# Performance work log

Hardware: AMD Instinct MI355X
Metric: run time of the kernel (lower is better)

The kernel has to match this reference:

```python
import jax, jax.numpy as jnp
import numpy as np

IN_F, RED, WID, CLS, T = 700, 256, 4096, 20, 100


def _q4(W):
    # per-tensor symmetric INT4 STE: value is quantized, grad is identity
    scale = jnp.maximum(jnp.abs(W).max() / 7.0, 1e-8)
    return W + jax.lax.stop_gradient(jnp.round(W / scale) * scale - W)


def setup_inputs() -> dict:
    key = jax.random.key(0)
    ks = jax.random.split(key, 12)
    B = 64
    x = jax.random.normal(ks[0], (B, T, IN_F), dtype=jnp.float32)
    latent = jax.random.uniform(ks[1], (T,), dtype=jnp.float32)
    spatial_W = jax.random.normal(ks[2], (RED, IN_F), jnp.float32) / np.sqrt(IN_F)
    spatial_b = jnp.zeros((RED,), jnp.float32)
    conv_W = jax.random.normal(ks[3], (RED, RED, 5), jnp.float32) / np.sqrt(RED * 5)
    conv_b = jnp.zeros((RED,), jnp.float32)
    fc1_W = jax.random.normal(ks[4], (WID, RED), jnp.float32) / np.sqrt(RED)
    fc1_b = jnp.zeros((WID,), jnp.float32)
    fc2_W = jax.random.normal(ks[5], (CLS, WID), jnp.float32) / np.sqrt(WID)
    fc2_b = jnp.zeros((CLS,), jnp.float32)
    gain = jnp.asarray(1.0, jnp.float32)
    return {"x": x, "latent": latent, "spatial_W": spatial_W, "spatial_b": spatial_b,
            "conv_W": conv_W, "conv_b": conv_b, "fc1_W": fc1_W, "fc1_b": fc1_b,
            "fc2_W": fc2_W, "fc2_b": fc2_b, "gain": gain}


def _compute_drive(x, latent, spatial_W, spatial_b, conv_W, conv_b, fc1_W, fc1_b, gain):
    # spatial projection (INT4 STE linear) + relu : (B,T,RED)
    xp = jax.nn.relu(jnp.einsum("btf,rf->btr", x, _q4(spatial_W)) + spatial_b)
    # temporal conv1d over T, padding=2 (same), channels RED->RED
    xc = jax.lax.conv_general_dilated(
        xp.transpose(0, 2, 1), conv_W, window_strides=(1,), padding=[(2, 2)],
        dimension_numbers=("NCH", "OIH", "NCH"))
    conv_out = jax.nn.relu(xc + conv_b[None, :, None]).transpose(0, 2, 1)  # (B,T,RED)
    spatial_act = jax.nn.softplus(jnp.einsum("btr,wr->btw", conv_out, _q4(fc1_W)) + fc1_b)
    return spatial_act * latent[None, :, None] * jnp.abs(gain)  # (B,T,WID)


def reference(x, latent, spatial_W, spatial_b, conv_W, conv_b, fc1_W, fc1_b, fc2_W, fc2_b, gain):
    drive = _compute_drive(x, latent, spatial_W, spatial_b, conv_W, conv_b, fc1_W, fc1_b, gain)
    # Poisson spike sampling with straight-through estimator, then clamp at 1
    pois = jax.random.poisson(jax.random.key(42), jax.lax.stop_gradient(drive)).astype(drive.dtype)
    spikes = drive + jax.lax.stop_gradient(pois - drive)
    spikes = jnp.minimum(spikes, 1.0)
    # decay-weighted temporal reduction over T
    decay = jnp.exp(jnp.linspace(-2.0, 0.0, T)).astype(drive.dtype)
    weighted = jnp.einsum("btw,t->bw", spikes, decay)  # (B,WID)
    # dropout in eval mode = identity
    logits = weighted @ _q4(fc2_W).T + fc2_b  # (B,CLS)
    return (logits, spikes, drive)
```

## Files before the change

kernel.cpp:

```cpp
#include <hip/hip_runtime.h>
#include <stdint.h>

#define B 64
#define T 100
#define IN_F 700
#define RED 256
#define WID 4096
#define CLS 20
#define BT (B*T)
#define NELEM (BT*WID)
#define LOGITS_OFF 0
#define SPIKES_OFF (B*CLS)
#define DRIVE_OFF (SPIKES_OFF + NELEM)

#define WS_SLOTS 0
#define WS_W2Q 16
#define WS_XP  (WS_W2Q + CLS*WID)
#define WS_CO  (WS_XP + BT*RED)
#define WS_WEIGHTED (WS_CO + BT*RED)

#define SC_WST 0
#define SC_CWT (SC_WST + IN_F*RED)

__host__ __device__ __forceinline__ uint32_t rotl32(uint32_t v, int r) {
  return (v << r) | (v >> (32 - r));
}

__host__ __device__ __forceinline__ void threefry2x32(uint32_t k0, uint32_t k1,
                                                      uint32_t x0, uint32_t x1,
                                                      uint32_t& o0, uint32_t& o1) {
  uint32_t k2 = k0 ^ k1 ^ 0x1BD11BDAu;
  x0 += k0; x1 += k1;
#define TF_R(r) { x0 += x1; x1 = rotl32(x1, (r)); x1 ^= x0; }
  TF_R(13) TF_R(15) TF_R(26) TF_R(6)
  x0 += k1; x1 += k2 + 1u;
  TF_R(17) TF_R(29) TF_R(16) TF_R(24)
  x0 += k2; x1 += k0 + 2u;
  TF_R(13) TF_R(15) TF_R(26) TF_R(6)
  x0 += k0; x1 += k1 + 3u;
  TF_R(17) TF_R(29) TF_R(16) TF_R(24)
  x0 += k1; x1 += k2 + 4u;
  TF_R(13) TF_R(15) TF_R(26) TF_R(6)
  x0 += k2; x1 += k0 + 5u;
#undef TF_R
  o0 = x0; o1 = x1;
}

__global__ void absmax_kernel(const float* __restrict__ w, int n, uint32_t* slot) {
  __shared__ uint32_t sm[256];
  uint32_t m = 0u;
  for (int i = blockIdx.x * 256 + threadIdx.x; i < n; i += gridDim.x * 256)
    m = max(m, __float_as_uint(fabsf(w[i])));
  sm[threadIdx.x] = m;
  __syncthreads();
  for (int s = 128; s > 0; s >>= 1) {
    if (threadIdx.x < s) sm[threadIdx.x] = max(sm[threadIdx.x], sm[threadIdx.x + s]);
    __syncthreads();
  }
  if (threadIdx.x == 0) atomicMax(slot, sm[0]);
}

__global__ void quant_t_kernel(const float* __restrict__ w, float* __restrict__ qT,
                               int Nn, int Kk, const uint32_t* __restrict__ slot) {
  float s = fmaxf(__uint_as_float(*slot) / 7.0f, 1e-8f);
  int id = blockIdx.x * 256 + threadIdx.x;
  if (id < Nn * Kk) {
    int n = id / Kk, k = id - n * Kk;
    qT[(size_t)k * Nn + n] = rintf(w[id] / s) * s;
  }
}

__global__ void quant_kernel(const float* __restrict__ w, float* __restrict__ q,
                             int n, const uint32_t* __restrict__ slot) {
  float s = fmaxf(__uint_as_float(*slot) / 7.0f, 1e-8f);
  int i = blockIdx.x * 256 + threadIdx.x;
  if (i < n) q[i] = rintf(w[i] / s) * s;
}

__global__ void convw_t_kernel(const float* __restrict__ w, float* __restrict__ wt) {
  int id = blockIdx.x * 256 + threadIdx.x;
  if (id < 256 * 1280) {
    int o = id / 1280, r = id - o * 1280;
    int ic = r / 5, h = r - ic * 5;
    wt[(size_t)((h << 8) + ic) * 256 + o] = w[id];
  }
}

template<int SRCA>
__global__ __launch_bounds__(256, 8)
void gemm64_kernel(const float* __restrict__ A, const float* __restrict__ Bt,
                   const float* __restrict__ bias, float* __restrict__ C,
                   int M, int N, int K) {
  constexpr int MT = 64, NT = 64, TM = 4, TN = 4;
  constexpr int ASR = MT + 4, BSR = NT + 4;
  __shared__ float As[32 * ASR];
  __shared__ float Bs[32 * BSR];
  int tid = threadIdx.x;
  int tx = tid & 15, ty = tid >> 4;
  int m0 = blockIdx.x * MT, n0 = blockIdx.y * NT;
  float acc[TM * TN];
#pragma unroll
  for (int i = 0; i < TM * TN; ++i) acc[i] = 0.f;

  for (int kt = 0; kt < K; kt += 32) {
    int klen = K - kt; if (klen > 32) klen = 32;
#pragma unroll
    for (int rep = 0; rep < 2; ++rep) {
      int e = rep * 256 + tid;
      int am = e >> 3, ak4 = (e & 7) << 2;
      float4 av = make_float4(0.f, 0.f, 0.f, 0.f);
      if (ak4 < klen) {
        if (SRCA == 0) {
          av = *(const float4*)&A[(size_t)(m0 + am) * K + kt + ak4];
        } else {
          int k = kt + ak4;
          int h = k >> 8, ic = k & 255;
          int bt = m0 + am;
          int b = bt / T, t = bt - b * T;
          int tt = t + h - 2;
          if (tt >= 0 && tt < T)
            av = *(const float4*)&A[((size_t)(b * T + tt)) * RED + ic];
        }
      }
      As[(ak4 + 0) * ASR + am] = av.x;
      As[(ak4 + 1) * ASR + am] = av.y;
      As[(ak4 + 2) * ASR + am] = av.z;
      As[(ak4 + 3) * ASR + am] = av.w;
    }
#pragma unroll
    for (int rep = 0; rep < 2; ++rep) {
      int e = rep * 256 + tid;
      int n4 = (e & 15) << 2, kk = e >> 4;
      float4 v = make_float4(0.f, 0.f, 0.f, 0.f);
      if (kk < klen) v = *(const float4*)&Bt[(size_t)(kt + kk) * N + n0 + n4];
      *(float4*)&Bs[kk * BSR + n4] = v;
    }
    __syncthreads();
    if (klen == 32) {
#pragma unroll
      for (int kk = 0; kk < 32; ++kk) {
        float a[TM], b[TN];
#pragma unroll
        for (int i = 0; i < TM; ++i) a[i] = As[kk * ASR + ty * TM + i];
#pragma unroll
        for (int d = 0; d < TN; ++d) b[d] = Bs[kk * BSR + tx * TN + d];
#pragma unroll
        for (int j = 0; j < TM; ++j)
#pragma unroll
          for (int d = 0; d < TN; ++d)
            acc[j * TN + d] = fmaf(a[j], b[d], acc[j * TN + d]);
      }
    } else {
      for (int kk = 0; kk < klen; ++kk) {
        float a[TM], b[TN];
#pragma unroll
        for (int i = 0; i < TM; ++i) a[i] = As[kk * ASR + ty * TM + i];
#pragma unroll
        for (int d = 0; d < TN; ++d) b[d] = Bs[kk * BSR + tx * TN + d];
#pragma unroll
        for (int j = 0; j < TM; ++j)
#pragma unroll
          for (int d = 0; d < TN; ++d)
            acc[j * TN + d] = fmaf(a[j], b[d], acc[j * TN + d]);
      }
    }
    __syncthreads();
  }

  float bv[TN];
#pragma unroll
  for (int d = 0; d < TN; ++d) bv[d] = bias[n0 + tx * TN + d];
#pragma unroll
  for (int j = 0; j < TM; ++j) {
    int m = m0 + ty * TM + j;
    float o[TN];
#pragma unroll
    for (int d = 0; d < TN; ++d) o[d] = fmaxf(acc[j * TN + d] + bv[d], 0.0f);
    *(float4*)&C[(size_t)m * N + n0 + tx * TN] = make_float4(o[0], o[1], o[2], o[3]);
  }
}

__global__ __launch_bounds__(256, 2)
void fc1_kernel(const float* __restrict__ A, const float* __restrict__ W1,
                const float* __restrict__ bias, const float* __restrict__ latent,
                const float* __restrict__ gain, float* __restrict__ C,
                const uint32_t* __restrict__ slot, int K, int N) {
  constexpr int MT = 128, NT = 128, TM = 8, TN = 8;
  constexpr int ASR = MT + 4, BSR = NT + 4;
  __shared__ float As[32 * ASR];
  __shared__ float Bs[32 * BSR];
  float qs = fmaxf(__uint_as_float(*slot) / 7.0f, 1e-8f);
  int tid = threadIdx.x;
  int tx = tid & 15, ty = tid >> 4;
  int wid = (blockIdx.x & 7) * 200 + (blockIdx.x >> 3);
  int bx = wid % 50, by = wid / 50;
  int m0 = bx * MT, n0 = by * NT;
  float acc[TM * TN];
#pragma unroll
  for (int i = 0; i < TM * TN; ++i) acc[i] = 0.f;

  for (int kt = 0; kt < K; kt += 32) {
#pragma unroll
    for (int rep = 0; rep < 4; ++rep) {
      int e = rep * 256 + tid;
      int k4 = (e & 7) << 2, m = e >> 3;
      const float4 v = *(const float4*)&A[(size_t)(m0 + m) * K + kt + k4];
      As[(k4 + 0) * ASR + m] = v.x;
      As[(k4 + 1) * ASR + m] = v.y;
      As[(k4 + 2) * ASR + m] = v.z;
      As[(k4 + 3) * ASR + m] = v.w;
    }
#pragma unroll
    for (int rep = 0; rep < 4; ++rep) {
      int e = rep * 256 + tid;
      int bn = e >> 3, k4 = (e & 7) << 2;
      const float4 v = *(const float4*)&W1[(size_t)(n0 + bn) * K + kt + k4];
      Bs[(k4 + 0) * BSR + bn] = rintf(v.x / qs) * qs;
      Bs[(k4 + 1) * BSR + bn] = rintf(v.y / qs) * qs;
      Bs[(k4 + 2) * BSR + bn] = rintf(v.z / qs) * qs;
      Bs[(k4 + 3) * BSR + bn] = rintf(v.w / qs) * qs;
    }
    __syncthreads();
#pragma unroll
    for (int kk = 0; kk < 32; ++kk) {
      float a[TM], b[TN];
#pragma unroll
      for (int i = 0; i < TM; ++i) a[i] = As[kk * ASR + ty * TM + i];
#pragma unroll
      for (int d = 0; d < 4; ++d) b[d] = Bs[kk * BSR + tx * 4 + d];
#pragma unroll
      for (int d = 0; d < 4; ++d) b[4 + d] = Bs[kk * BSR + 64 + tx * 4 + d];
#pragma unroll
      for (int j = 0; j < TM; ++j)
#pragma unroll
        for (int d = 0; d < TN; ++d)
          acc[j * TN + d] = fmaf(a[j], b[d], acc[j * TN + d]);
    }
    __syncthreads();
  }

  float g = fabsf(gain[0]);
  float bv[TN];
#pragma unroll
  for (int d = 0; d < 4; ++d) {
    bv[d] = bias[n0 + tx * 4 + d];
    bv[4 + d] = bias[n0 + 64 + tx * 4 + d];
  }
#pragma unroll
  for (int j = 0; j < TM; ++j) {
    int bt = m0 + ty * TM + j;
    int q = bt / T;
    float lat = latent[bt - q * T];
    float o[TN];
#pragma unroll
    for (int d = 0; d < TN; ++d) {
      float v = acc[j * TN + d] + bv[d];
      float e = expf(-fabsf(v));
      float l = log1pf(e);
      float sp = fmaxf(v, 0.0f) + l;
      o[d] = (sp * lat) * g;
    }
    float4 o0 = make_float4(o[0], o[1], o[2], o[3]);
    float4 o1 = make_float4(o[4], o[5], o[6], o[7]);
    *(float4*)&C[(size_t)bt * N + n0 + tx * 4] = o0;
    *(float4*)&C[(size_t)bt * N + n0 + 64 + tx * 4] = o1;
  }
}

__global__ __launch_bounds__(256) void spike_weighted_kernel(float* __restrict__ out,
                                                             float* __restrict__ wt,
                                                             uint32_t k0, uint32_t k1) {
  __shared__ float dec[128];
  int tid = threadIdx.x;
  if (tid < T) {
    float step = 2.0f / 99.0f;
    float a = step * (float)tid;
    dec[tid] = expf(a - 2.0f);
  }
  __syncthreads();
  int b = blockIdx.x >> 4;
  int w = ((blockIdx.x & 15) << 8) + tid;
  float acc = 0.f;
  for (int t = 0; t < T; ++t) {
    uint32_t p = (uint32_t)((b * T + t) * WID + w);
    float lam = out[DRIVE_OFF + p];
    uint32_t y0, y1;
    threefry2x32(k0, k1, 0u, p, y0, y1);
    uint32_t bits = y0 ^ y1;
    float u = __uint_as_float((bits >> 9) | 0x3f800000u) - 1.0f;
    float s = (lam > 0.0f && logf(u) > -lam) ? 1.0f : 0.0f;
    out[SPIKES_OFF + p] = s;
    acc = fmaf(s, dec[t], acc);
  }
  wt[b * WID + w] = acc;
}

__global__ void logits_kernel(const float* __restrict__ wt,
                              const float* __restrict__ w2,
                              const float* __restrict__ b2,
                              float* __restrict__ out) {
  __shared__ float sm[256];
  int b = blockIdx.x / CLS, c = blockIdx.x - b * CLS;
  const float* wr = wt + (size_t)b * WID;
  const float* w2r = w2 + (size_t)c * WID;
  float p = 0.f;
  for (int w = threadIdx.x; w < WID; w += 256) p = fmaf(wr[w], w2r[w], p);
  sm[threadIdx.x] = p;
  __syncthreads();
  for (int s = 128; s > 0; s >>= 1) {
    if (threadIdx.x < s) sm[threadIdx.x] += sm[threadIdx.x + s];
    __syncthreads();
  }
  if (threadIdx.x == 0) out[LOGITS_OFF + blockIdx.x] = sm[0] + b2[c];
}

extern "C" void kernel_launch(void* const* d_in, const int* in_sizes, int n_in,
                              void* d_out, int out_size, void* d_ws, size_t ws_size,
                              hipStream_t stream) {
  (void)in_sizes; (void)n_in; (void)out_size; (void)ws_size;
  const float* x         = (const float*)d_in[0];
  const float* latent    = (const float*)d_in[1];
  const float* spatial_W = (const float*)d_in[2];
  const float* spatial_b = (const float*)d_in[3];
  const float* conv_W    = (const float*)d_in[4];
  const float* conv_b    = (const float*)d_in[5];
  const float* fc1_W     = (const float*)d_in[6];
  const float* fc1_b     = (const float*)d_in[7];
  const float* fc2_W     = (const float*)d_in[8];
  const float* fc2_b     = (const float*)d_in[9];
  const float* gain      = (const float*)d_in[10];
  float* out = (float*)d_out;
  uint32_t* wsu = (uint32_t*)d_ws;
  float* wsf = (float*)d_ws;
  float* S = out + SPIKES_OFF;

  uint32_t sk0, sk1;
  threefry2x32(0u, 42u, 0u, 1u, sk0, sk1);

  hipMemsetAsync(wsu + WS_SLOTS, 0, 3 * sizeof(uint32_t), stream);
  absmax_kernel<<<64, 256, 0, stream>>>(spatial_W, RED * IN_F, wsu + WS_SLOTS + 0);
  absmax_kernel<<<256, 256, 0, stream>>>(fc1_W, WID * RED, wsu + WS_SLOTS + 1);
  absmax_kernel<<<32, 256, 0, stream>>>(fc2_W, CLS * WID, wsu + WS_SLOTS + 2);

  quant_t_kernel<<<700, 256, 0, stream>>>(spatial_W, S + SC_WST, RED, IN_F, wsu + WS_SLOTS + 0);
  quant_kernel<<<320, 256, 0, stream>>>(fc2_W, wsf + WS_W2Q, wsu ? CLS * WID : 0, wsu + WS_SLOTS + 2);
  convw_t_kernel<<<1280, 256, 0, stream>>>(conv_W, S + SC_CWT);

  gemm64_kernel<0><<<dim3(100, 4), 256, 0, stream>>>(
      x, S + SC_WST, spatial_b, wsf + WS_XP, BT, RED, IN_F);

  gemm64_kernel<1><<<dim3(100, 4), 256, 0, stream>>>(
      wsf + WS_XP, S + SC_CWT, conv_b, wsf + WS_CO, BT, RED, 1280);

  fc1_kernel<<<1600, 256, 0, stream>>>(
      wsf + WS_CO, fc1_W, fc1_b, latent, gain, out + DRIVE_OFF,
      wsu + WS_SLOTS + 1, RED, WID);

  spike_weighted_kernel<<<B * 16, 256, 0, stream>>>(out, wsf + WS_WEIGHTED, sk0, sk1);

  logits_kernel<<<B * CLS, 256, 0, stream>>>(wsf + WS_WEIGHTED, wsf + WS_W2Q, fc2_b, out);
}
```

Baseline: 752.9 us.

## Fuse Poisson spike sampling and decay-weighted reduction into fc1 GEMM epilogue

The fc1 GEMM epilogue now generates spikes with threefry directly from the in-register drive values, writes both drive and spikes, and accumulates decay-weighted sums. These partial sums are reduced per block in LDS and added into a zeroed workspace with atomics. This removes the separate spike kernel, which re-read the entire 105 MB drive tensor. The K tile shrinks to 16 and launch bounds rise to 4 blocks per CU to lower LDS use and raise occupancy. In exchange the epilogue gets heavier, float atomics make the summation order nondeterministic, and an extra memset is added.

```diff
diff --git a/kernel.cpp b/kernel.cpp
--- a/kernel.cpp
+++ b/kernel.cpp
@@ -180,119 +180,138 @@
   }
 }
 
-__global__ __launch_bounds__(256, 2)
-void fc1_kernel(const float* __restrict__ A, const float* __restrict__ W1,
-                const float* __restrict__ bias, const float* __restrict__ latent,
-                const float* __restrict__ gain, float* __restrict__ C,
-                const uint32_t* __restrict__ slot, int K, int N) {
-  constexpr int MT = 128, NT = 128, TM = 8, TN = 8;
-  constexpr int ASR = MT + 4, BSR = NT + 4;
-  __shared__ float As[32 * ASR];
-  __shared__ float Bs[32 * BSR];
+__global__ __launch_bounds__(256, 4)
+void fc1_fused_kernel(const float* __restrict__ A, const float* __restrict__ W1,
+                      const float* __restrict__ bias, const float* __restrict__ latent,
+                      const float* __restrict__ gain, float* __restrict__ drive,
+                      float* __restrict__ spikes, float* __restrict__ wtacc,
+                      const uint32_t* __restrict__ slot,
+                      uint32_t k0, uint32_t k1) {
+  constexpr int KT_ = 16, ASR = 132, BSR = 132;
+  __shared__ float lds[KT_ * ASR + KT_ * BSR];
+  float* As = lds;
+  float* Bs = lds + KT_ * ASR;
   float qs = fmaxf(__uint_as_float(*slot) / 7.0f, 1e-8f);
   int tid = threadIdx.x;
   int tx = tid & 15, ty = tid >> 4;
   int wid = (blockIdx.x & 7) * 200 + (blockIdx.x >> 3);
   int bx = wid % 50, by = wid / 50;
-  int m0 = bx * MT, n0 = by * NT;
-  float acc[TM * TN];
-#pragma unroll
-  for (int i = 0; i < TM * TN; ++i) acc[i] = 0.f;
-
-  for (int kt = 0; kt < K; kt += 32) {
-#pragma unroll
-    for (int rep = 0; rep < 4; ++rep) {
-      int e = rep * 256 + tid;
-      int k4 = (e & 7) << 2, m = e >> 3;
-      const float4 v = *(const float4*)&A[(size_t)(m0 + m) * K + kt + k4];
-      As[(k4 + 0) * ASR + m] = v.x;
-      As[(k4 + 1) * ASR + m] = v.y;
-      As[(k4 + 2) * ASR + m] = v.z;
-      As[(k4 + 3) * ASR + m] = v.w;
-    }
-#pragma unroll
-    for (int rep = 0; rep < 4; ++rep) {
-      int e = rep * 256 + tid;
-      int bn = e >> 3, k4 = (e & 7) << 2;
-      const float4 v = *(const float4*)&W1[(size_t)(n0 + bn) * K + kt + k4];
-      Bs[(k4 + 0) * BSR + bn] = rintf(v.x / qs) * qs;
-      Bs[(k4 + 1) * BSR + bn] = rintf(v.y / qs) * qs;
-      Bs[(k4 + 2) * BSR + bn] = rintf(v.z / qs) * qs;
-      Bs[(k4 + 3) * BSR + bn] = rintf(v.w / qs) * qs;
-    }
-    __syncthreads();
-#pragma unroll
-    for (int kk = 0; kk < 32; ++kk) {
-      float a[TM], b[TN];
-#pragma unroll
-      for (int i = 0; i < TM; ++i) a[i] = As[kk * ASR + ty * TM + i];
+  int m0 = bx * 128, n0 = by * 128;
+  int am = tid >> 2, ak4 = (tid & 3) << 2;
+  float acc[64];
+#pragma unroll
+  for (int i = 0; i < 64; ++i) acc[i] = 0.f;
+
+  for (int kt = 0; kt < RED; kt += KT_) {
+#pragma unroll
+    for (int rep = 0; rep < 2; ++rep) {
+      int m = rep * 64 + am;
+      const float4 v = *(const float4*)&A[(size_t)(m0 + m) * RED + kt + ak4];
+      As[(ak4 + 0) * ASR + m] = v.x;
+      As[(ak4 + 1) * ASR + m] = v.y;
+      As[(ak4 + 2) * ASR + m] = v.z;
+      As[(ak4 + 3) * ASR + m] = v.w;
+    }
+#pragma unroll
+    for (int rep = 0; rep < 2; ++rep) {
+      int bn = rep * 64 + am;
+      const float4 v = *(const float4*)&W1[(size_t)(n0 + bn) * RED + kt + ak4];
+      Bs[(ak4 + 0) * BSR + bn] = rintf(v.x / qs) * qs;
+      Bs[(ak4 + 1) * BSR + bn] = rintf(v.y / qs) * qs;
+      Bs[(ak4 + 2) * BSR + bn] = rintf(v.z / qs) * qs;
+      Bs[(ak4 + 3) * BSR + bn] = rintf(v.w / qs) * qs;
+    }
+    __syncthreads();
+#pragma unroll
+    for (int kk = 0; kk < KT_; ++kk) {
+      float a[8], b[8];
+#pragma unroll
+      for (int i = 0; i < 8; ++i) a[i] = As[kk * ASR + ty * 8 + i];
 #pragma unroll
       for (int d = 0; d < 4; ++d) b[d] = Bs[kk * BSR + tx * 4 + d];
 #pragma unroll
       for (int d = 0; d < 4; ++d) b[4 + d] = Bs[kk * BSR + 64 + tx * 4 + d];
 #pragma unroll
-      for (int j = 0; j < TM; ++j)
-#pragma unroll
-        for (int d = 0; d < TN; ++d)
-          acc[j * TN + d] = fmaf(a[j], b[d], acc[j * TN + d]);
+      for (int j = 0; j < 8; ++j)
+#pragma unroll
+        for (int d = 0; d < 8; ++d)
+          acc[j * 8 + d] = fmaf(a[j], b[d], acc[j * 8 + d]);
     }
     __syncthreads();
   }
 
   float g = fabsf(gain[0]);
-  float bv[TN];
+  float bv[8];
 #pragma unroll
   for (int d = 0; d < 4; ++d) {
     bv[d] = bias[n0 + tx * 4 + d];
     bv[4 + d] = bias[n0 + 64 + tx * 4 + d];
   }
-#pragma unroll
-  for (int j = 0; j < TM; ++j) {
-    int bt = m0 + ty * TM + j;
+  int bA = m0 / T;
+  int qFirst = (m0 + ty * 8) / T;
+  float wA[8], wB[8];
+#pragma unroll
+  for (int d = 0; d < 8; ++d) { wA[d] = 0.f; wB[d] = 0.f; }
+
+#pragma unroll
+  for (int j = 0; j < 8; ++j) {
+    int bt = m0 + ty * 8 + j;
     int q = bt / T;
-    float lat = latent[bt - q * T];
-    float o[TN];
-#pragma unroll
-    for (int d = 0; d < TN; ++d) {
-      float v = acc[j * TN + d] + bv[d];
+    int t = bt - q * T;
+    float lat = latent[t];
+    float dec = expf((2.0f / 99.0f) * (float)t - 2.0f);
+    float o[8];
+#pragma unroll
+    for (int d = 0; d < 8; ++d) {
+      float v = acc[j * 8 + d] + bv[d];
       float e = expf(-fabsf(v));
       float l = log1pf(e);
-      float sp = fmaxf(v, 0.0f) + l;
-      o[d] = (sp * lat) * g;
-    }
-    float4 o0 = make_float4(o[0], o[1], o[2], o[3]);
-    float4 o1 = make_float4(o[4], o[5], o[6], o[7]);
-    *(float4*)&C[(size_t)bt * N + n0 + tx * 4] = o0;
-    *(float4*)&C[(size_t)bt * N + n0 + 64 + tx * 4] = o1;
-  }
-}
-
-__global__ __launch_bounds__(256) void spike_weighted_kernel(float* __restrict__ out,
-                                                             float* __restrict__ wt,
-                                                             uint32_t k0, uint32_t k1) {
-  __shared__ float dec[128];
-  int tid = threadIdx.x;
-  if (tid < T) {
-    float step = 2.0f / 99.0f;
-    float a = step * (float)tid;
-    dec[tid] = expf(a - 2.0f);
-  }
+      float sp_ = fmaxf(v, 0.0f) + l;
+      o[d] = (sp_ * lat) * g;
+    }
+    size_t row = (size_t)bt * WID + n0;
+    *(float4*)&drive[row + tx * 4]      = make_float4(o[0], o[1], o[2], o[3]);
+    *(float4*)&drive[row + 64 + tx * 4] = make_float4(o[4], o[5], o[6], o[7]);
+    float sp[8];
+    bool isA = (q == qFirst);
+#pragma unroll
+    for (int d = 0; d < 8; ++d) {
+      int n = n0 + ((d < 4) ? (tx * 4 + d) : (64 + tx * 4 + d - 4));
+      uint32_t p = (uint32_t)(bt * WID + n);
+      uint32_t y0, y1;
+      threefry2x32(k0, k1, 0u, p, y0, y1);
+      uint32_t bits = y0 ^ y1;
+      float u = __uint_as_float((bits >> 9) | 0x3f800000u) - 1.0f;
+      float s = (o[d] > 0.0f && logf(u) > -o[d]) ? 1.0f : 0.0f;
+      sp[d] = s;
+      float c = s * dec;
+      if (isA) wA[d] += c; else wB[d] += c;
+    }
+    *(float4*)&spikes[row + tx * 4]      = make_float4(sp[0], sp[1], sp[2], sp[3]);
+    *(float4*)&spikes[row + 64 + tx * 4] = make_float4(sp[4], sp[5], sp[6], sp[7]);
+  }
+
   __syncthreads();
-  int b = blockIdx.x >> 4;
-  int w = ((blockIdx.x & 15) << 8) + tid;
-  float acc = 0.f;
-  for (int t = 0; t < T; ++t) {
-    uint32_t p = (uint32_t)((b * T + t) * WID + w);
-    float lam = out[DRIVE_OFF + p];
-    uint32_t y0, y1;
-    threefry2x32(k0, k1, 0u, p, y0, y1);
-    uint32_t bits = y0 ^ y1;
-    float u = __uint_as_float((bits >> 9) | 0x3f800000u) - 1.0f;
-    float s = (lam > 0.0f && logf(u) > -lam) ? 1.0f : 0.0f;
-    out[SPIKES_OFF + p] = s;
-    acc = fmaf(s, dec[t], acc);
-  }
-  wt[b * WID + w] = acc;
+  float* red = lds;
+  for (int bb = 0; bb < 3; ++bb) {
+    int btarget = bA + bb;
+    if (btarget * T > m0 + 127) break;
+#pragma unroll
+    for (int d = 0; d < 4; ++d) {
+      float vlo = (qFirst == btarget) ? wA[d] : ((qFirst + 1 == btarget) ? wB[d] : 0.f);
+      float vhi = (qFirst == btarget) ? wA[4 + d] : ((qFirst + 1 == btarget) ? wB[4 + d] : 0.f);
+      red[ty * 128 + tx * 4 + d] = vlo;
+      red[ty * 128 + 64 + tx * 4 + d] = vhi;
+    }
+    __syncthreads();
+    if (tid < 128) {
+      float s = 0.f;
+#pragma unroll
+      for (int yy = 0; yy < 16; ++yy) s += red[yy * 128 + tid];
+      if (s != 0.f) atomicAdd(&wtacc[(size_t)btarget * WID + n0 + tid], s);
+    }
+    __syncthreads();
+  }
 }
 
 __global__ void logits_kernel(const float* __restrict__ wt,
@@ -338,12 +357,13 @@
   threefry2x32(0u, 42u, 0u, 1u, sk0, sk1);
 
   hipMemsetAsync(wsu + WS_SLOTS, 0, 3 * sizeof(uint32_t), stream);
+  hipMemsetAsync(wsf + WS_WEIGHTED, 0, (size_t)B * WID * sizeof(float), stream);
   absmax_kernel<<<64, 256, 0, stream>>>(spatial_W, RED * IN_F, wsu + WS_SLOTS + 0);
   absmax_kernel<<<256, 256, 0, stream>>>(fc1_W, WID * RED, wsu + WS_SLOTS + 1);
   absmax_kernel<<<32, 256, 0, stream>>>(fc2_W, CLS * WID, wsu + WS_SLOTS + 2);
 
   quant_t_kernel<<<700, 256, 0, stream>>>(spatial_W, S + SC_WST, RED, IN_F, wsu + WS_SLOTS + 0);
-  quant_kernel<<<320, 256, 0, stream>>>(fc2_W, wsf + WS_W2Q, wsu ? CLS * WID : 0, wsu + WS_SLOTS + 2);
+  quant_kernel<<<320, 256, 0, stream>>>(fc2_W, wsf + WS_W2Q, CLS * WID, wsu + WS_SLOTS + 2);
   convw_t_kernel<<<1280, 256, 0, stream>>>(conv_W, S + SC_CWT);
 
   gemm64_kernel<0><<<dim3(100, 4), 256, 0, stream>>>(
@@ -352,11 +372,10 @@
   gemm64_kernel<1><<<dim3(100, 4), 256, 0, stream>>>(
       wsf + WS_XP, S + SC_CWT, conv_b, wsf + WS_CO, BT, RED, 1280);
 
-  fc1_kernel<<<1600, 256, 0, stream>>>(
-      wsf + WS_CO, fc1_W, fc1_b, latent, gain, out + DRIVE_OFF,
-      wsu + WS_SLOTS + 1, RED, WID);
-
-  spike_weighted_kernel<<<B * 16, 256, 0, stream>>>(out, wsf + WS_WEIGHTED, sk0, sk1);
+  fc1_fused_kernel<<<1600, 256, 0, stream>>>(
+      wsf + WS_CO, fc1_W, fc1_b, latent, gain,
+      out + DRIVE_OFF, out + SPIKES_OFF, wsf + WS_WEIGHTED,
+      wsu + WS_SLOTS + 1, sk0, sk1);
 
   logits_kernel<<<B * CLS, 256, 0, stream>>>(wsf + WS_WEIGHTED, wsf + WS_W2Q, fc2_b, out);
 }
```

Result: no change. 761.8 us (+1.2%).
